# Optimization experiments

Measured on AMD Instinct MI355X. Metric: run time of the kernel, lower is better.

The kernel has to match this reference:

```python
import jax, jax.numpy as jnp
import numpy as np

C = 32          # channel multiplicity (uvu)
SQRT3 = float(np.sqrt(3.0))
SQRT2 = float(np.sqrt(2.0))


def setup_inputs() -> dict:
    key = jax.random.key(0)
    k1, k2, k3, k4, k5 = jax.random.split(key, 5)
    V, E = 50000, 800000
    X = jax.random.normal(k1, (V, 4 * C), dtype=jnp.float32)      # 32x0e + 32x1e
    Y = jax.random.normal(k2, (E, 4), dtype=jnp.float32)          # 0e + 1e edge harmonics
    W = jax.random.normal(k3, (E, 5 * C), dtype=jnp.float32)      # per-edge weights, 5 CG paths x C
    rows = jax.random.randint(k4, (E,), 0, V, dtype=jnp.int64)    # receiver node i
    cols = jax.random.randint(k5, (E,), 0, V, dtype=jnp.int64)    # sender node j
    return {"X": X, "Y": Y, "W": W, "rows": rows, "cols": cols}


def reference(X, Y, W, rows, cols):
    V = X.shape[0]
    E = Y.shape[0]
    # split node features into scalar (l=0) and vector (l=1) channels
    x0 = X[:, :C]                       # [V, C]
    x1 = X[:, C:].reshape(V, C, 3)      # [V, C, 3]
    # gather sender features per edge
    xj0 = x0[cols]                      # [E, C]
    xj1 = x1[cols]                      # [E, C, 3]
    y0 = Y[:, 0]                        # [E]
    y1 = Y[:, 1:4]                      # [E, 3]
    w = W.reshape(E, 5, C)
    # CG paths (channelwise 'uvu'):
    # 0e x 0e -> 0e
    p00 = w[:, 0] * xj0 * y0[:, None]                                   # [E, C]
    # 0e x 1e -> 1e
    p01 = (w[:, 1] * xj0)[:, :, None] * y1[:, None, :]                  # [E, C, 3]
    # 1e x 0e -> 1e
    p10 = (w[:, 2] * y0[:, None])[:, :, None] * xj1                    # [E, C, 3]
    # 1e x 1e -> 0e  (normalized dot product)
    p110 = w[:, 3] * jnp.einsum('eck,ek->ec', xj1, y1) / SQRT3          # [E, C]
    # 1e x 1e -> 1e  (normalized cross product)
    cross = jnp.cross(xj1, y1[:, None, :])                              # [E, C, 3]
    p111 = w[:, 4][:, :, None] * cross / SQRT2                          # [E, C, 3]
    out_e = jnp.concatenate([
        p00,
        p01.reshape(E, 3 * C),
        p10.reshape(E, 3 * C),
        p110,
        p111.reshape(E, 3 * C),
    ], axis=1)                                                          # [E, 11*C]
    # scatter-add messages into receiver nodes
    Z = jax.ops.segment_sum(out_e, rows, num_segments=V)                # [V, 11*C]
    return Z
```

## Files before the change

### kernel.cpp

```cpp
#include <hip/hip_runtime.h>
#include <hip/hip_bf16.h>


#define C 32
#define ZCOLS (11 * C)
#define MAXDEG 64
#define OVF_MAX 65536
#define INV_SQRT3 0.57735026918962576451f
#define INV_SQRT2 0.70710678118654752440f

__global__ void hist_scatter(const int* __restrict__ rows,
                             int* __restrict__ cnt,
                             int* __restrict__ bucket,
                             int* __restrict__ ovf_cnt,
                             int* __restrict__ ovf_list,
                             int E) {
    int e = blockIdx.x * blockDim.x + threadIdx.x;
    if (e >= E) return;
    int r = rows[e];
    int k = atomicAdd(&cnt[r], 1);
    if (k < MAXDEG) {
        bucket[(size_t)r * MAXDEG + k] = e;
    } else {
        int o = atomicAdd(ovf_cnt, 1);
        if (o < OVF_MAX) ovf_list[o] = e;
    }
}

__global__ void tpconv_rows(const float* __restrict__ X,
                            const float* __restrict__ Y,
                            const float* __restrict__ W,
                            const int* __restrict__ cols,
                            const int* __restrict__ cnt,
                            const int* __restrict__ bucket,
                            float* __restrict__ Z,
                            int V) {
    int wid  = blockIdx.x * (blockDim.x >> 6) + (threadIdx.x >> 6);
    int lane = threadIdx.x & 63;
    if (wid >= V) return;
    const int c = lane & 31;
    const int h = lane >> 5;

    int n = cnt[wid];
    if (n > MAXDEG) n = MAXDEG;

    float acc[11];
#pragma unroll
    for (int j = 0; j < 11; ++j) acc[j] = 0.0f;

    const int* bkt = bucket + (size_t)wid * MAXDEG;
    for (int i = h; i < n; i += 2) {
        const int e = bkt[i];
        const float4 y = *reinterpret_cast<const float4*>(Y + (size_t)e * 4);
        const int col = cols[e];

        const float* Xe = X + (size_t)col * (4 * C);
        const float xj0 = Xe[c];
        const float a0  = Xe[C + 3 * c + 0];
        const float a1  = Xe[C + 3 * c + 1];
        const float a2  = Xe[C + 3 * c + 2];

        const float* We = W + (size_t)e * (5 * C);
        const float w0 = We[0 * C + c];
        const float w1 = We[1 * C + c];
        const float w2 = We[2 * C + c];
        const float w3 = We[3 * C + c];
        const float w4 = We[4 * C + c];

        acc[0] += w0 * xj0 * y.x;

        const float t01 = w1 * xj0;
        acc[1] += t01 * y.y;
        acc[2] += t01 * y.z;
        acc[3] += t01 * y.w;

        const float t10 = w2 * y.x;
        acc[4] += t10 * a0;
        acc[5] += t10 * a1;
        acc[6] += t10 * a2;

        acc[7] += w3 * (a0 * y.y + a1 * y.z + a2 * y.w) * INV_SQRT3;

        const float s = w4 * INV_SQRT2;
        acc[8]  += s * (a1 * y.w - a2 * y.z);
        acc[9]  += s * (a2 * y.y - a0 * y.w);
        acc[10] += s * (a0 * y.z - a1 * y.y);
    }

#pragma unroll
    for (int j = 0; j < 11; ++j) acc[j] += __shfl_xor(acc[j], 32);

    if (h == 0) {
        float* Zr = Z + (size_t)wid * ZCOLS;
        Zr[c]               = acc[0];
        Zr[C + 3 * c + 0]   = acc[1];
        Zr[C + 3 * c + 1]   = acc[2];
        Zr[C + 3 * c + 2]   = acc[3];
        Zr[4 * C + 3 * c + 0] = acc[4];
        Zr[4 * C + 3 * c + 1] = acc[5];
        Zr[4 * C + 3 * c + 2] = acc[6];
        Zr[7 * C + c]       = acc[7];
        Zr[8 * C + 3 * c + 0] = acc[8];
        Zr[8 * C + 3 * c + 1] = acc[9];
        Zr[8 * C + 3 * c + 2] = acc[10];
    }
}

__global__ void ovf_apply(const float* __restrict__ X,
                          const float* __restrict__ Y,
                          const float* __restrict__ W,
                          const int* __restrict__ rows,
                          const int* __restrict__ cols,
                          const int* __restrict__ ovf_cnt,
                          const int* __restrict__ ovf_list,
                          float* __restrict__ Z) {
    int no = *ovf_cnt;
    if (no > OVF_MAX) no = OVF_MAX;
    int total = no * C;
    for (int t = blockIdx.x * blockDim.x + threadIdx.x; t < total;
         t += gridDim.x * blockDim.x) {
        const int i = t >> 5, c = t & 31;
        const int e = ovf_list[i];
        const float4 y = *reinterpret_cast<const float4*>(Y + (size_t)e * 4);
        const int row = rows[e];
        const int col = cols[e];
        const float* Xe = X + (size_t)col * (4 * C);
        const float xj0 = Xe[c];
        const float a0  = Xe[C + 3 * c + 0];
        const float a1  = Xe[C + 3 * c + 1];
        const float a2  = Xe[C + 3 * c + 2];
        const float* We = W + (size_t)e * (5 * C);
        const float w0 = We[c], w1 = We[C + c], w2 = We[2 * C + c],
                    w3 = We[3 * C + c], w4 = We[4 * C + c];
        float* Zr = Z + (size_t)row * ZCOLS;
        atomicAdd(&Zr[c], w0 * xj0 * y.x);
        const float t01 = w1 * xj0;
        atomicAdd(&Zr[C + 3 * c + 0], t01 * y.y);
        atomicAdd(&Zr[C + 3 * c + 1], t01 * y.z);
        atomicAdd(&Zr[C + 3 * c + 2], t01 * y.w);
        const float t10 = w2 * y.x;
        atomicAdd(&Zr[4 * C + 3 * c + 0], t10 * a0);
        atomicAdd(&Zr[4 * C + 3 * c + 1], t10 * a1);
        atomicAdd(&Zr[4 * C + 3 * c + 2], t10 * a2);
        atomicAdd(&Zr[7 * C + c], w3 * (a0 * y.y + a1 * y.z + a2 * y.w) * INV_SQRT3);
        const float s = w4 * INV_SQRT2;
        atomicAdd(&Zr[8 * C + 3 * c + 0], s * (a1 * y.w - a2 * y.z));
        atomicAdd(&Zr[8 * C + 3 * c + 1], s * (a2 * y.y - a0 * y.w));
        atomicAdd(&Zr[8 * C + 3 * c + 2], s * (a0 * y.z - a1 * y.y));
    }
}

extern "C" void kernel_launch(void* const* d_in, const int* in_sizes, int n_in,
                              void* d_out, int out_size, void* d_ws, size_t ws_size,
                              hipStream_t stream) {
    const float* X    = (const float*)d_in[0];
    const float* Y    = (const float*)d_in[1];
    const float* W    = (const float*)d_in[2];
    const int*   rows = (const int*)d_in[3];
    const int*   cols = (const int*)d_in[4];
    float*       Z    = (float*)d_out;

    const int E = in_sizes[1] / 4;
    const int V = in_sizes[0] / (4 * C);

    int* cnt      = (int*)d_ws;
    int* ovf_cnt  = cnt + V;
    int* ovf_list = ovf_cnt + 1;
    int* bucket   = ovf_list + OVF_MAX;

    hipMemsetAsync(cnt, 0, (size_t)(V + 1) * sizeof(int), stream);

    {
        const int threads = 256;
        const int blocks = (E + threads - 1) / threads;
        hist_scatter<<<blocks, threads, 0, stream>>>(rows, cnt, bucket, ovf_cnt,
                                                     ovf_list, E);
    }
    {
        const int threads = 256;
        const int wavesPerBlock = threads / 64;
        const int blocks = (V + wavesPerBlock - 1) / wavesPerBlock;
        tpconv_rows<<<blocks, threads, 0, stream>>>(X, Y, W, cols, cnt, bucket, Z, V);
    }
    {
        ovf_apply<<<64, 256, 0, stream>>>(X, Y, W, rows, cols, ovf_cnt, ovf_list, Z);
    }
}
```

Before: 224.2 us.

## Store edge/col pairs in buckets, persistent waves with prefetch and shuffle broadcast

The histogram kernel now stores the sender column next to each edge id in the bucket, which removes the dependent cols[e] lookup from the gather kernel. The gather kernel becomes persistent: a fixed grid of 1536 blocks strides over rows and prefetches the next row's count and bucket entries. Each lane loads one bucket entry up front, and the entries are broadcast with shuffles instead of being reloaded. Two edges per half-wave are processed per iteration to expose more memory-level parallelism, at the cost of a larger bucket array (8 bytes per slot) and more writes in the histogram step.

```diff
diff --git a/kernel.cpp b/kernel.cpp
--- a/kernel.cpp
+++ b/kernel.cpp
@@ -9,9 +9,12 @@
 #define INV_SQRT3 0.57735026918962576451f
 #define INV_SQRT2 0.70710678118654752440f
 
+struct alignas(8) EdgeCol { int e; int c; };
+
 __global__ void hist_scatter(const int* __restrict__ rows,
+                             const int* __restrict__ cols,
                              int* __restrict__ cnt,
-                             int* __restrict__ bucket,
+                             EdgeCol* __restrict__ bucket,
                              int* __restrict__ ovf_cnt,
                              int* __restrict__ ovf_list,
                              int E) {
@@ -20,7 +23,10 @@
     int r = rows[e];
     int k = atomicAdd(&cnt[r], 1);
     if (k < MAXDEG) {
-        bucket[(size_t)r * MAXDEG + k] = e;
+        EdgeCol p;
+        p.e = e;
+        p.c = cols[e];
+        bucket[(size_t)r * MAXDEG + k] = p;
     } else {
         int o = atomicAdd(ovf_cnt, 1);
         if (o < OVF_MAX) ovf_list[o] = e;
@@ -30,79 +36,106 @@
 __global__ void tpconv_rows(const float* __restrict__ X,
                             const float* __restrict__ Y,
                             const float* __restrict__ W,
-                            const int* __restrict__ cols,
                             const int* __restrict__ cnt,
-                            const int* __restrict__ bucket,
+                            const EdgeCol* __restrict__ bucket,
                             float* __restrict__ Z,
                             int V) {
-    int wid  = blockIdx.x * (blockDim.x >> 6) + (threadIdx.x >> 6);
-    int lane = threadIdx.x & 63;
-    if (wid >= V) return;
+    const int nwaves = (gridDim.x * blockDim.x) >> 6;
+    const int wave   = (blockIdx.x * blockDim.x + threadIdx.x) >> 6;
+    const int lane   = threadIdx.x & 63;
     const int c = lane & 31;
     const int h = lane >> 5;
 
-    int n = cnt[wid];
-    if (n > MAXDEG) n = MAXDEG;
-
-    float acc[11];
+    if (wave >= V) return;
+
+    int n_cur = cnt[wave];
+    EdgeCol p_cur = bucket[(size_t)wave * MAXDEG + lane];
+
+    for (int row = wave; row < V; row += nwaves) {
+        const int row_nxt = row + nwaves;
+        int n_nxt = 0;
+        EdgeCol p_nxt;
+        p_nxt.e = 0; p_nxt.c = 0;
+        if (row_nxt < V) {
+            n_nxt = cnt[row_nxt];
+            p_nxt = bucket[(size_t)row_nxt * MAXDEG + lane];
+        }
+
+        int n = n_cur;
+        if (n > MAXDEG) n = MAXDEG;
+        int eb = p_cur.e;
+        int cb = p_cur.c;
+
+        float acc[11];
 #pragma unroll
-    for (int j = 0; j < 11; ++j) acc[j] = 0.0f;
-
-    const int* bkt = bucket + (size_t)wid * MAXDEG;
-    for (int i = h; i < n; i += 2) {
-        const int e = bkt[i];
-        const float4 y = *reinterpret_cast<const float4*>(Y + (size_t)e * 4);
-        const int col = cols[e];
-
-        const float* Xe = X + (size_t)col * (4 * C);
-        const float xj0 = Xe[c];
-        const float a0  = Xe[C + 3 * c + 0];
-        const float a1  = Xe[C + 3 * c + 1];
-        const float a2  = Xe[C + 3 * c + 2];
-
-        const float* We = W + (size_t)e * (5 * C);
-        const float w0 = We[0 * C + c];
-        const float w1 = We[1 * C + c];
-        const float w2 = We[2 * C + c];
-        const float w3 = We[3 * C + c];
-        const float w4 = We[4 * C + c];
-
-        acc[0] += w0 * xj0 * y.x;
-
-        const float t01 = w1 * xj0;
-        acc[1] += t01 * y.y;
-        acc[2] += t01 * y.z;
-        acc[3] += t01 * y.w;
-
-        const float t10 = w2 * y.x;
-        acc[4] += t10 * a0;
-        acc[5] += t10 * a1;
-        acc[6] += t10 * a2;
-
-        acc[7] += w3 * (a0 * y.y + a1 * y.z + a2 * y.w) * INV_SQRT3;
-
-        const float s = w4 * INV_SQRT2;
-        acc[8]  += s * (a1 * y.w - a2 * y.z);
-        acc[9]  += s * (a2 * y.y - a0 * y.w);
-        acc[10] += s * (a0 * y.z - a1 * y.y);
-    }
+        for (int j = 0; j < 11; ++j) acc[j] = 0.0f;
+
+        auto body = [&](int e, int col) {
+            const float4 y = *reinterpret_cast<const float4*>(Y + (size_t)e * 4);
+
+            const float* Xe = X + (size_t)col * (4 * C);
+            const float xj0 = Xe[c];
+            const float a0  = Xe[C + 3 * c + 0];
+            const float a1  = Xe[C + 3 * c + 1];
+            const float a2  = Xe[C + 3 * c + 2];
+
+            const float* We = W + (size_t)e * (5 * C);
+            const float w0 = We[0 * C + c];
+            const float w1 = We[1 * C + c];
+            const float w2 = We[2 * C + c];
+            const float w3 = We[3 * C + c];
+            const float w4 = We[4 * C + c];
+
+            acc[0] += w0 * xj0 * y.x;
+
+            const float t01 = w1 * xj0;
+            acc[1] += t01 * y.y;
+            acc[2] += t01 * y.z;
+            acc[3] += t01 * y.w;
+
+            const float t10 = w2 * y.x;
+            acc[4] += t10 * a0;
+            acc[5] += t10 * a1;
+            acc[6] += t10 * a2;
+
+            acc[7] += w3 * (a0 * y.y + a1 * y.z + a2 * y.w) * INV_SQRT3;
+
+            const float s = w4 * INV_SQRT2;
+            acc[8]  += s * (a1 * y.w - a2 * y.z);
+            acc[9]  += s * (a2 * y.y - a0 * y.w);
+            acc[10] += s * (a0 * y.z - a1 * y.y);
+        };
+
+        const int jmax = (n + 3) >> 2;
+        for (int j = 0; j < jmax; ++j) {
+            const int ia = 4 * j + h;
+            const int ib = ia + 2;
+            const int ea = __shfl(eb, ia), ca = __shfl(cb, ia);
+            const int e2 = __shfl(eb, ib), c2 = __shfl(cb, ib);
+            if (ia < n) body(ea, ca);
+            if (ib < n) body(e2, c2);
+        }
 
 #pragma unroll
-    for (int j = 0; j < 11; ++j) acc[j] += __shfl_xor(acc[j], 32);
-
-    if (h == 0) {
-        float* Zr = Z + (size_t)wid * ZCOLS;
-        Zr[c]               = acc[0];
-        Zr[C + 3 * c + 0]   = acc[1];
-        Zr[C + 3 * c + 1]   = acc[2];
-        Zr[C + 3 * c + 2]   = acc[3];
-        Zr[4 * C + 3 * c + 0] = acc[4];
-        Zr[4 * C + 3 * c + 1] = acc[5];
-        Zr[4 * C + 3 * c + 2] = acc[6];
-        Zr[7 * C + c]       = acc[7];
-        Zr[8 * C + 3 * c + 0] = acc[8];
-        Zr[8 * C + 3 * c + 1] = acc[9];
-        Zr[8 * C + 3 * c + 2] = acc[10];
+        for (int j = 0; j < 11; ++j) acc[j] += __shfl_xor(acc[j], 32);
+
+        if (h == 0) {
+            float* Zr = Z + (size_t)row * ZCOLS;
+            Zr[c]                 = acc[0];
+            Zr[C + 3 * c + 0]     = acc[1];
+            Zr[C + 3 * c + 1]     = acc[2];
+            Zr[C + 3 * c + 2]     = acc[3];
+            Zr[4 * C + 3 * c + 0] = acc[4];
+            Zr[4 * C + 3 * c + 1] = acc[5];
+            Zr[4 * C + 3 * c + 2] = acc[6];
+            Zr[7 * C + c]         = acc[7];
+            Zr[8 * C + 3 * c + 0] = acc[8];
+            Zr[8 * C + 3 * c + 1] = acc[9];
+            Zr[8 * C + 3 * c + 2] = acc[10];
+        }
+
+        n_cur = n_nxt;
+        p_cur = p_nxt;
     }
 }
 
@@ -163,24 +196,23 @@
     const int E = in_sizes[1] / 4;
     const int V = in_sizes[0] / (4 * C);
 
-    int* cnt      = (int*)d_ws;
-    int* ovf_cnt  = cnt + V;
-    int* ovf_list = ovf_cnt + 1;
-    int* bucket   = ovf_list + OVF_MAX;
+    EdgeCol* bucket   = (EdgeCol*)d_ws;
+    int*     cnt      = (int*)(bucket + (size_t)V * MAXDEG);
+    int*     ovf_cnt  = cnt + V;
+    int*     ovf_list = ovf_cnt + 1;
 
     hipMemsetAsync(cnt, 0, (size_t)(V + 1) * sizeof(int), stream);
 
     {
         const int threads = 256;
         const int blocks = (E + threads - 1) / threads;
-        hist_scatter<<<blocks, threads, 0, stream>>>(rows, cnt, bucket, ovf_cnt,
-                                                     ovf_list, E);
+        hist_scatter<<<blocks, threads, 0, stream>>>(rows, cols, cnt, bucket,
+                                                     ovf_cnt, ovf_list, E);
     }
     {
         const int threads = 256;
-        const int wavesPerBlock = threads / 64;
-        const int blocks = (V + wavesPerBlock - 1) / wavesPerBlock;
-        tpconv_rows<<<blocks, threads, 0, stream>>>(X, Y, W, cols, cnt, bucket, Z, V);
+        const int blocks = 1536;
+        tpconv_rows<<<blocks, threads, 0, stream>>>(X, Y, W, cnt, bucket, Z, V);
     }
     {
         ovf_apply<<<64, 256, 0, stream>>>(X, Y, W, rows, cols, ovf_cnt, ovf_list, Z);
```

New measurement: 224.0 us. Within noise of the previous version (-0.1%).
